# Performance work log

Hardware: AMD Instinct MI355X
Metric: run time of the kernel (lower is better)

Reference implementation:

```python
import jax, jax.numpy as jnp
import numpy as np

P_SIZE = 13
B_THRESH = 1.3  # |u| >= b -> hard 1.0
N_POW = 64      # u^n / (u^n + 1)


def make_dct_weight(p):
    idx = np.arange(p)
    Ci = np.where(idx == 0, 1.0 / np.sqrt(2.0), 1.0)
    cos = np.cos((2 * idx[:, None] + 1) * idx[None, :] * np.pi / (2 * p)) * Ci[None, :]  # [x,i]
    P = (2.0 / p) * np.einsum('xi,yj->xyij', cos, cos).reshape(p * p, p * p)
    return P.T.astype(np.float32).reshape(p * p, 1, p, p)


def conv2d(x, w, padding):
    return jax.lax.conv_general_dilated(x, w, (1, 1), padding,
                                        dimension_numbers=('NCHW', 'OIHW', 'NCHW'))


def udiff(u):
    # x^64/(x^64+1), saturated to 1 for |x| >= 1.3 (even power, sign-safe)
    au = jnp.abs(u)
    us = jnp.where(au < B_THRESH, u, 0.0)  # avoid overflow in pow
    y = us ** N_POW
    return jnp.where(au >= B_THRESH, jnp.ones_like(u), y / (y + 1.0))


def setup_inputs() -> dict:
    key = jax.random.key(0)
    k1, _ = jax.random.split(key)
    x = jax.random.uniform(k1, (2, 1, 512, 512), dtype=jnp.float32)
    sigma = jnp.full((1,), 0.1, dtype=jnp.float32)
    W_dct = jnp.asarray(make_dct_weight(P_SIZE))  # [p^2, 1, p, p], learnable in original
    return {"x": x, "sigma": sigma, "W_dct": W_dct}


def reference(x, sigma, W_dct):
    N, _, H, W = x.shape
    p = W_dct.shape[-1]
    pp = p * p
    # patch DCT: [N, p^2, H-p+1, W-p+1]
    t = conv2d(x, W_dct, 'VALID')
    nz = udiff(t / (3.0 * sigma))
    y = t * nz
    w = 1.0 / (1.0 + jnp.sum(nz, axis=1, keepdims=True))  # [N,1,H',W']
    # inverse transform as 1x1 conv with inv(dct matrix)
    Minv = jnp.linalg.inv(W_dct.reshape(pp, pp))
    z = jnp.einsum('kc,nchw->nkhw', Minv, y)
    z = w * z
    # overlap-add fold == conv with spatially-flipped identity patch kernel, full padding
    fold_k = jnp.flip(jnp.eye(pp, dtype=x.dtype).reshape(pp, p, p), axis=(1, 2))[None]  # [1,p^2,p,p]
    folded = conv2d(z, fold_k, [(p - 1, p - 1), (p - 1, p - 1)])  # [N,1,H,W]
    out = folded[:, :, p - 1:H - (p - 1), p - 1:W - (p - 1)]
    divisor = conv2d(w, jnp.ones((1, 1, p, p), x.dtype), 'VALID')
    return out / divisor
```

## Files before the change

kernel.cpp:

```cpp
#include <hip/hip_runtime.h>
#include <math.h>


#define P13    13
#define IMGW   512
#define OUTW   488
#define SEGH   31
#define NSEG   16
#define HCOLS  512
#define HPITCH 16

struct C1mat { float v[P13 * P13]; };

constexpr double kPI = 3.14159265358979323846264338327950288;

constexpr double ccos_pm_pi(double th) {
    double term = 1.0, s = 1.0;
    const double th2 = th * th;
    for (int n = 1; n <= 25; ++n) {
        term *= -th2 / (double)((2 * n - 1) * (2 * n));
        s += term;
    }
    return s;
}
constexpr double csqrt(double v) {
    double x = (v > 1.0) ? v : 1.0;
    for (int i = 0; i < 64; ++i) x = 0.5 * (x + v / x);
    return x;
}
constexpr C1mat make_c1() {
    C1mat m{};
    const double s213 = csqrt(2.0 / 13.0);
    const double is2  = 1.0 / csqrt(2.0);
    for (int x = 0; x < P13; ++x)
        for (int k = 0; k < P13; ++k) {
            int mm = ((2 * x + 1) * k) % 52;
            double th = (mm <= 26) ? (mm * kPI / 26.0) : ((mm - 52) * kPI / 26.0);
            double Ci = (k == 0) ? is2 : 1.0;
            m.v[x * P13 + k] = (float)(s213 * Ci * ccos_pm_pi(th));
        }
    return m;
}
__device__ constexpr C1mat c1c = make_c1();

struct FalseT { static constexpr bool value = false; };
struct TrueT  { static constexpr bool value = true; };

#define ROR16_ADD(v, N)                                                        \
    v += __int_as_float(__builtin_amdgcn_mov_dpp(__float_as_int(v),            \
                                                 0x120 + (N), 0xF, 0xF, true))

__device__ __forceinline__ void vdct_shrink(const float (&Rv)[P13],
                                            float inv3s, float (&tn)[P13], float& pnz)
{
    float Se[6], So[6];
#pragma unroll
    for (int k = 0; k < 6; ++k) { Se[k] = Rv[k] + Rv[12 - k]; So[k] = Rv[k] - Rv[12 - k]; }
#pragma unroll
    for (int i = 0; i < P13; ++i) {
        float t;
        if ((i & 1) == 0) {
            t = c1c.v[6 * P13 + i] * Rv[6];
#pragma unroll
            for (int k = 0; k < 6; ++k) t = fmaf(c1c.v[k * P13 + i], Se[k], t);
        } else {
            t = c1c.v[0 * P13 + i] * So[0];
#pragma unroll
            for (int k = 1; k < 6; ++k) t = fmaf(c1c.v[k * P13 + i], So[k], t);
        }
        float u = t * inv3s;
        float lg = __builtin_amdgcn_logf(fabsf(u));
        float q  = __builtin_amdgcn_exp2f(-64.0f * lg);
        float nz = __builtin_amdgcn_rcpf(1.0f + q);
        pnz += nz;
        tn[i] = t * nz;
    }
}

__device__ __forceinline__ void fold_vert(const float (&tn)[P13], float w1, float (&H)[P13])
{
#pragma unroll
    for (int dx = 0; dx < 6; ++dx) {
        float E = c1c.v[dx * P13 + 0] * tn[0];
#pragma unroll
        for (int i = 2; i < P13; i += 2) E = fmaf(c1c.v[dx * P13 + i], tn[i], E);
        float O = c1c.v[dx * P13 + 1] * tn[1];
#pragma unroll
        for (int i = 3; i < P13; i += 2) O = fmaf(c1c.v[dx * P13 + i], tn[i], O);
        H[dx]      = fmaf(w1, E + O, H[dx]);
        H[12 - dx] = fmaf(w1, E - O, H[12 - dx]);
    }
    float z6 = c1c.v[6 * P13 + 0] * tn[0];
#pragma unroll
    for (int i = 2; i < P13; i += 2) z6 = fmaf(c1c.v[6 * P13 + i], tn[i], z6);
    H[6] = fmaf(w1, z6, H[6]);
}

__global__ __launch_bounds__(256) void dct2net_k2(
    const float* __restrict__ xg, const float* __restrict__ sigmag,
    float* __restrict__ Hg, float* __restrict__ Wg)
{
    __shared__ float c1lds[169];
    const int tid = threadIdx.x;
    if (tid < 169) c1lds[tid] = c1c.v[tid];
    __syncthreads();

    const int lane = tid & 63;
    const int wv   = tid >> 6;
    const int g    = lane >> 4;
    const int jj   = lane & 15;
    const int img  = blockIdx.z;
    const int hs   = blockIdx.y * SEGH;
    const int segrows = (OUTW - hs < SEGH) ? (OUTW - hs) : SEGH;
    const int cbw  = blockIdx.x * 16 + wv * 4;
    const int col  = cbw + g;

    const float inv3s = 1.0f / (3.0f * sigmag[0]);
    const float* xin  = xg + (size_t)img * IMGW * IMGW;

    float c1col[P13];
    {
        const int jc = (jj < 13) ? jj : 12;
#pragma unroll
        for (int y = 0; y < P13; ++y) c1col[y] = c1lds[y * P13 + jc];
    }

    float Rv[P13], Hr[P13], wr[12];
#pragma unroll
    for (int k = 0; k < P13; ++k) { Rv[k] = 0.0f; Hr[k] = 0.0f; }
#pragma unroll
    for (int k = 0; k < 12; ++k) wr[k] = 0.0f;
    float vs = 0.0f;

    int xcol = cbw + lane; xcol = (xcol < IMGW - 1) ? xcol : (IMGW - 1);
    float xv = 0.0f;
    if (lane < 16) xv = xin[(size_t)hs * IMGW + xcol];

    auto step = [&](int k, auto SH, auto RT) {
        float xw[P13];
#pragma unroll
        for (int y = 0; y < P13; ++y)
            xw[y] = __int_as_float(
                __builtin_amdgcn_ds_bpermute(4 * (g + y), __float_as_int(xv)));
        {
            int nr = hs + k + 1; nr = (nr < IMGW) ? nr : (IMGW - 1);
            if (lane < 16) xv = xin[(size_t)nr * IMGW + xcol];
        }
        float a0 = c1col[0] * xw[0], a1 = c1col[1] * xw[1];
#pragma unroll
        for (int y = 2; y < P13; y += 2) a0 = fmaf(c1col[y], xw[y], a0);
#pragma unroll
        for (int y = 3; y < P13; y += 2) a1 = fmaf(c1col[y], xw[y], a1);
#pragma unroll
        for (int q = 0; q < P13 - 1; ++q) Rv[q] = Rv[q + 1];
        Rv[P13 - 1] = a0 + a1;

        if constexpr (decltype(SH)::value) {
            float tn[P13]; float pnz = 0.0f;
            vdct_shrink(Rv, inv3s, tn, pnz);
            if (jj >= 13) pnz = 0.0f;
            ROR16_ADD(pnz, 1);
            ROR16_ADD(pnz, 2);
            ROR16_ADD(pnz, 4);
            ROR16_ADD(pnz, 8);
            const float w = __builtin_amdgcn_rcpf(1.0f + pnz);
            vs += w;
            fold_vert(tn, w, Hr);
            if constexpr (decltype(RT)::value) {
                const int a = hs + k - 24;
                Hg[(((size_t)img * OUTW + a) * HCOLS + col) * HPITCH + jj] = Hr[0];
                if (jj == 0) Wg[((size_t)img * IMGW + a) * IMGW + col] = vs;
                vs -= wr[0];
            }
#pragma unroll
            for (int q = 0; q < 11; ++q) wr[q] = wr[q + 1];
            wr[11] = w;
#pragma unroll
            for (int q = 0; q < P13 - 1; ++q) Hr[q] = Hr[q + 1];
            Hr[P13 - 1] = 0.0f;
        }
    };

#pragma unroll 4
    for (int k = 0; k < 12; ++k) step(k, FalseT{}, FalseT{});
#pragma unroll 4
    for (int k = 12; k < 24; ++k) step(k, TrueT{}, FalseT{});
    const int kend = 24 + segrows;
#pragma unroll 4
    for (int k = 24; k < kend; ++k) step(k, TrueT{}, TrueT{});
}

__global__ __launch_bounds__(256) void dct2net_k3(
    const float* __restrict__ Hg, const float* __restrict__ Wg,
    float* __restrict__ outg)
{
    __shared__ float U[4][76][14];
    __shared__ float vw[4][80];
    const int tid  = threadIdx.x;
    const int lane = tid & 63;
    const int wv   = tid >> 6;
    const int img  = blockIdx.z;
    const int a    = blockIdx.y * 4 + wv;
    const int cb   = blockIdx.x * 64;

#pragma unroll
    for (int h = 0; h < 2; ++h) {
        const int li = lane + 64 * h;
        if (h == 0 || lane < 12) {
            int c = cb + li; c = (c < 499) ? c : 499;
            const float* hp = &Hg[(((size_t)img * OUTW + a) * HCOLS + c) * HPITCH];
            float hv[P13];
            *(float4*)&hv[0] = *(const float4*)hp;
            *(float4*)&hv[4] = *(const float4*)(hp + 4);
            *(float4*)&hv[8] = *(const float4*)(hp + 8);
            hv[12] = hp[12];
            vw[wv][li] = Wg[((size_t)img * IMGW + a) * IMGW + c];
#pragma unroll
            for (int dy = 0; dy < P13; ++dy) {
                float s0 = c1c.v[dy * P13 + 0] * hv[0];
                float s1 = c1c.v[dy * P13 + 1] * hv[1];
#pragma unroll
                for (int j = 2; j < P13; j += 2) s0 = fmaf(c1c.v[dy * P13 + j], hv[j], s0);
#pragma unroll
                for (int j = 3; j < P13; j += 2) s1 = fmaf(c1c.v[dy * P13 + j], hv[j], s1);
                U[wv][li][dy] = s0 + s1;
            }
        }
    }
    float num = 0.0f;
#pragma unroll
    for (int dy = 0; dy < P13; ++dy) num += U[wv][lane + 12 - dy][dy];
    float den = 0.0f;
#pragma unroll
    for (int d = 0; d < P13; ++d) den += vw[wv][lane + d];
    const int ow = cb + lane;
    if (ow < OUTW)
        outg[((size_t)img * OUTW + a) * OUTW + ow] = num * __builtin_amdgcn_rcpf(den);
}

extern "C" void kernel_launch(void* const* d_in, const int* in_sizes, int n_in,
                              void* d_out, int out_size, void* d_ws, size_t ws_size,
                              hipStream_t stream)
{
    const float* x     = (const float*)d_in[0];
    const float* sigma = (const float*)d_in[1];
    float* out = (float*)d_out;

    float* Hg = (float*)d_ws;
    float* Wg = Hg + (size_t)2 * OUTW * HCOLS * HPITCH;

    dct2net_k2<<<dim3(32, NSEG, 2), 256, 0, stream>>>(x, sigma, Hg, Wg);
    dct2net_k3<<<dim3(8, 122, 2), 256, 0, stream>>>(Hg, Wg, out);
}
```

Measured before the change: 179.9 us.

## Rotate register rings, square-power shrink, 64-thread k2 blocks, spread k3 halo

Kernel k2 now runs as single-wave blocks with taller segments. The steady-state loop is unrolled 13 times with compile-time rotating register indices, so the per-row shift of the Rv/Hr/wr arrays goes away, and pointers advance incrementally. The shrink function replaces log/exp2 with repeated squaring of t^2/(9s^2), clamped at 1.69, and computes 1-nz directly. In k3, the 12-column halo work is spread across 48 threads instead of making lanes 0-11 of every wave do two passes, and a __syncthreads is added. Risks include higher register pressure, a different numerical path for the shrink weight, and fewer halo-recompute segments being traded for fewer, larger blocks.

```diff
diff --git a/kernel.cpp b/kernel.cpp
--- a/kernel.cpp
+++ b/kernel.cpp
@@ -5,8 +5,8 @@
 #define P13    13
 #define IMGW   512
 #define OUTW   488
-#define SEGH   31
-#define NSEG   16
+#define SEGH   39
+#define NSEG   13
 #define HCOLS  512
 #define HPITCH 16
 
@@ -50,17 +50,22 @@
     v += __int_as_float(__builtin_amdgcn_mov_dpp(__float_as_int(v),            \
                                                  0x120 + (N), 0xF, 0xF, true))
 
-__device__ __forceinline__ void vdct_shrink(const float (&Rv)[P13],
-                                            float inv3s, float (&tn)[P13], float& pnz)
+template<int RO>
+__device__ __forceinline__ void vdct_shrink_r(const float (&Rv)[P13], float i2sq,
+                                              float (&tn)[P13], float& pnzr)
 {
     float Se[6], So[6];
 #pragma unroll
-    for (int k = 0; k < 6; ++k) { Se[k] = Rv[k] + Rv[12 - k]; So[k] = Rv[k] - Rv[12 - k]; }
+    for (int k = 0; k < 6; ++k) {
+        float a = Rv[(k + RO) % P13], b = Rv[(12 - k + RO) % P13];
+        Se[k] = a + b; So[k] = a - b;
+    }
+    const float R6v = Rv[(6 + RO) % P13];
 #pragma unroll
     for (int i = 0; i < P13; ++i) {
         float t;
         if ((i & 1) == 0) {
-            t = c1c.v[6 * P13 + i] * Rv[6];
+            t = c1c.v[6 * P13 + i] * R6v;
 #pragma unroll
             for (int k = 0; k < 6; ++k) t = fmaf(c1c.v[k * P13 + i], Se[k], t);
         } else {
@@ -68,16 +73,17 @@
 #pragma unroll
             for (int k = 1; k < 6; ++k) t = fmaf(c1c.v[k * P13 + i], So[k], t);
         }
-        float u = t * inv3s;
-        float lg = __builtin_amdgcn_logf(fabsf(u));
-        float q  = __builtin_amdgcn_exp2f(-64.0f * lg);
-        float nz = __builtin_amdgcn_rcpf(1.0f + q);
-        pnz += nz;
-        tn[i] = t * nz;
-    }
-}
-
-__device__ __forceinline__ void fold_vert(const float (&tn)[P13], float w1, float (&H)[P13])
+        float p2 = fminf(t * t * i2sq, 1.69f);
+        float p4 = p2 * p2, p8 = p4 * p4, p16 = p8 * p8, p32 = p16 * p16, p64 = p32 * p32;
+        float r  = __builtin_amdgcn_rcpf(p64 + 1.0f);
+        pnzr += r;
+        tn[i] = fmaf(-t, r, t);
+    }
+}
+
+template<int R>
+__device__ __forceinline__ void fold_vert_r(const float (&tn)[P13], float w1,
+                                            float (&H)[P13])
 {
 #pragma unroll
     for (int dx = 0; dx < 6; ++dx) {
@@ -87,65 +93,105 @@
         float O = c1c.v[dx * P13 + 1] * tn[1];
 #pragma unroll
         for (int i = 3; i < P13; i += 2) O = fmaf(c1c.v[dx * P13 + i], tn[i], O);
-        H[dx]      = fmaf(w1, E + O, H[dx]);
-        H[12 - dx] = fmaf(w1, E - O, H[12 - dx]);
+        H[(dx + R) % P13]      = fmaf(w1, E + O, H[(dx + R) % P13]);
+        H[(12 - dx + R) % P13] = fmaf(w1, E - O, H[(12 - dx + R) % P13]);
     }
     float z6 = c1c.v[6 * P13 + 0] * tn[0];
 #pragma unroll
     for (int i = 2; i < P13; i += 2) z6 = fmaf(c1c.v[6 * P13 + i], tn[i], z6);
-    H[6] = fmaf(w1, z6, H[6]);
-}
-
-__global__ __launch_bounds__(256) void dct2net_k2(
+    H[(6 + R) % P13] = fmaf(w1, z6, H[(6 + R) % P13]);
+}
+
+template<int R>
+__device__ __forceinline__ void k2_sub(
+    float (&Rv)[P13], float (&Hr)[P13], float (&wr)[P13],
+    float& vs, float& xv, const float*& xp, const float* xlast, int xcol,
+    const float (&c1col)[P13], int g, int jj, float i2sq,
+    float*& Hp, float*& Wp, int voH, int voW)
+{
+    float xw[P13];
+#pragma unroll
+    for (int y = 0; y < P13; ++y)
+        xw[y] = __int_as_float(
+            __builtin_amdgcn_ds_bpermute(4 * (g + y), __float_as_int(xv)));
+    {
+        const float* xq = (xp < xlast) ? xp : xlast;
+        xv = xq[xcol]; xp += IMGW;
+    }
+    float a0 = c1col[0] * xw[0], a1 = c1col[1] * xw[1];
+#pragma unroll
+    for (int y = 2; y < P13; y += 2) a0 = fmaf(c1col[y], xw[y], a0);
+#pragma unroll
+    for (int y = 3; y < P13; y += 2) a1 = fmaf(c1col[y], xw[y], a1);
+    Rv[R] = a0 + a1;
+
+    float tn[P13]; float pnzr = 0.0f;
+    vdct_shrink_r<(R + 1) % P13>(Rv, i2sq, tn, pnzr);
+    float pnz = 13.0f - pnzr;
+    ROR16_ADD(pnz, 1); ROR16_ADD(pnz, 2); ROR16_ADD(pnz, 4); ROR16_ADD(pnz, 8);
+    const float w = __builtin_amdgcn_rcpf(1.0f + pnz);
+    vs += w;
+    fold_vert_r<R>(tn, w, Hr);
+    wr[R] = w;
+    Hp[voH] = Hr[R];
+    Hp += HCOLS * HPITCH;
+    if (jj == 0) Wp[voW] = vs;
+    Wp += IMGW;
+    vs -= wr[(R + 1) % P13];
+    Hr[R] = 0.0f;
+}
+
+__global__ __launch_bounds__(64) void dct2net_k2(
     const float* __restrict__ xg, const float* __restrict__ sigmag,
     float* __restrict__ Hg, float* __restrict__ Wg)
 {
     __shared__ float c1lds[169];
     const int tid = threadIdx.x;
-    if (tid < 169) c1lds[tid] = c1c.v[tid];
-    __syncthreads();
-
-    const int lane = tid & 63;
-    const int wv   = tid >> 6;
+    c1lds[tid] = c1c.v[tid];
+    c1lds[tid + 64] = c1c.v[tid + 64];
+    if (tid < 41) c1lds[tid + 128] = c1c.v[tid + 128];
+
+    const int lane = tid;
     const int g    = lane >> 4;
     const int jj   = lane & 15;
     const int img  = blockIdx.z;
     const int hs   = blockIdx.y * SEGH;
     const int segrows = (OUTW - hs < SEGH) ? (OUTW - hs) : SEGH;
-    const int cbw  = blockIdx.x * 16 + wv * 4;
+    const int cbw  = blockIdx.x * 4;
     const int col  = cbw + g;
 
     const float inv3s = 1.0f / (3.0f * sigmag[0]);
+    const float i2sq  = inv3s * inv3s;
     const float* xin  = xg + (size_t)img * IMGW * IMGW;
 
     float c1col[P13];
-    {
-        const int jc = (jj < 13) ? jj : 12;
-#pragma unroll
-        for (int y = 0; y < P13; ++y) c1col[y] = c1lds[y * P13 + jc];
-    }
-
-    float Rv[P13], Hr[P13], wr[12];
-#pragma unroll
-    for (int k = 0; k < P13; ++k) { Rv[k] = 0.0f; Hr[k] = 0.0f; }
-#pragma unroll
-    for (int k = 0; k < 12; ++k) wr[k] = 0.0f;
+#pragma unroll
+    for (int y = 0; y < P13; ++y)
+        c1col[y] = (jj < 13) ? c1lds[y * P13 + jj] : 0.0f;
+
+    float Rv[P13], Hr[P13], wr[P13];
+#pragma unroll
+    for (int k = 0; k < P13; ++k) { Rv[k] = 0.0f; Hr[k] = 0.0f; wr[k] = 0.0f; }
     float vs = 0.0f;
 
-    int xcol = cbw + lane; xcol = (xcol < IMGW - 1) ? xcol : (IMGW - 1);
-    float xv = 0.0f;
-    if (lane < 16) xv = xin[(size_t)hs * IMGW + xcol];
-
-    auto step = [&](int k, auto SH, auto RT) {
+    int xcol = cbw + (lane & 15); xcol = (xcol < IMGW - 1) ? xcol : (IMGW - 1);
+    const float* xp    = xin + (size_t)hs * IMGW;
+    const float* xlast = xin + (size_t)(IMGW - 1) * IMGW;
+    float xv = xp[xcol];
+    xp += IMGW;
+
+    float* Hp = Hg + ((size_t)img * OUTW + hs) * HCOLS * HPITCH;
+    float* Wp = Wg + ((size_t)img * IMGW + hs) * IMGW;
+    const int voH = col * HPITCH + jj;
+    const int voW = col;
+
+    auto stepS = [&](auto SH, auto RT) {
         float xw[P13];
 #pragma unroll
         for (int y = 0; y < P13; ++y)
             xw[y] = __int_as_float(
                 __builtin_amdgcn_ds_bpermute(4 * (g + y), __float_as_int(xv)));
-        {
-            int nr = hs + k + 1; nr = (nr < IMGW) ? nr : (IMGW - 1);
-            if (lane < 16) xv = xin[(size_t)nr * IMGW + xcol];
-        }
+        { const float* xq = (xp < xlast) ? xp : xlast; xv = xq[xcol]; xp += IMGW; }
         float a0 = c1col[0] * xw[0], a1 = c1col[1] * xw[1];
 #pragma unroll
         for (int y = 2; y < P13; y += 2) a0 = fmaf(c1col[y], xw[y], a0);
@@ -156,38 +202,46 @@
         Rv[P13 - 1] = a0 + a1;
 
         if constexpr (decltype(SH)::value) {
-            float tn[P13]; float pnz = 0.0f;
-            vdct_shrink(Rv, inv3s, tn, pnz);
-            if (jj >= 13) pnz = 0.0f;
-            ROR16_ADD(pnz, 1);
-            ROR16_ADD(pnz, 2);
-            ROR16_ADD(pnz, 4);
-            ROR16_ADD(pnz, 8);
+            float tn[P13]; float pnzr = 0.0f;
+            vdct_shrink_r<0>(Rv, i2sq, tn, pnzr);
+            float pnz = 13.0f - pnzr;
+            ROR16_ADD(pnz, 1); ROR16_ADD(pnz, 2); ROR16_ADD(pnz, 4); ROR16_ADD(pnz, 8);
             const float w = __builtin_amdgcn_rcpf(1.0f + pnz);
             vs += w;
-            fold_vert(tn, w, Hr);
+            fold_vert_r<0>(tn, w, Hr);
+#pragma unroll
+            for (int q = 0; q < P13 - 1; ++q) wr[q] = wr[q + 1];
+            wr[P13 - 1] = w;
             if constexpr (decltype(RT)::value) {
-                const int a = hs + k - 24;
-                Hg[(((size_t)img * OUTW + a) * HCOLS + col) * HPITCH + jj] = Hr[0];
-                if (jj == 0) Wg[((size_t)img * IMGW + a) * IMGW + col] = vs;
+                Hp[voH] = Hr[0];
+                Hp += HCOLS * HPITCH;
+                if (jj == 0) Wp[voW] = vs;
+                Wp += IMGW;
                 vs -= wr[0];
             }
 #pragma unroll
-            for (int q = 0; q < 11; ++q) wr[q] = wr[q + 1];
-            wr[11] = w;
-#pragma unroll
             for (int q = 0; q < P13 - 1; ++q) Hr[q] = Hr[q + 1];
             Hr[P13 - 1] = 0.0f;
         }
     };
 
-#pragma unroll 4
-    for (int k = 0; k < 12; ++k) step(k, FalseT{}, FalseT{});
-#pragma unroll 4
-    for (int k = 12; k < 24; ++k) step(k, TrueT{}, FalseT{});
-    const int kend = 24 + segrows;
-#pragma unroll 4
-    for (int k = 24; k < kend; ++k) step(k, TrueT{}, TrueT{});
+#pragma unroll 1
+    for (int k = 0; k < 12; ++k) stepS(FalseT{}, FalseT{});
+#pragma unroll 1
+    for (int k = 0; k < 12; ++k) stepS(TrueT{}, FalseT{});
+
+#define SUB(R) k2_sub<R>(Rv, Hr, wr, vs, xv, xp, xlast, xcol, c1col, g, jj, \
+                         i2sq, Hp, Wp, voH, voW)
+    int kleft = segrows;
+#pragma unroll 1
+    while (kleft >= 13) {
+        SUB(0); SUB(1); SUB(2); SUB(3); SUB(4); SUB(5); SUB(6);
+        SUB(7); SUB(8); SUB(9); SUB(10); SUB(11); SUB(12);
+        kleft -= 13;
+    }
+#undef SUB
+#pragma unroll 1
+    for (; kleft > 0; --kleft) stepS(TrueT{}, TrueT{});
 }
 
 __global__ __launch_bounds__(256) void dct2net_k3(
@@ -200,33 +254,66 @@
     const int lane = tid & 63;
     const int wv   = tid >> 6;
     const int img  = blockIdx.z;
-    const int a    = blockIdx.y * 4 + wv;
+    const int a0   = blockIdx.y * 4;
+    const int a    = a0 + wv;
     const int cb   = blockIdx.x * 64;
 
-#pragma unroll
-    for (int h = 0; h < 2; ++h) {
-        const int li = lane + 64 * h;
-        if (h == 0 || lane < 12) {
-            int c = cb + li; c = (c < 499) ? c : 499;
-            const float* hp = &Hg[(((size_t)img * OUTW + a) * HCOLS + c) * HPITCH];
-            float hv[P13];
-            *(float4*)&hv[0] = *(const float4*)hp;
-            *(float4*)&hv[4] = *(const float4*)(hp + 4);
-            *(float4*)&hv[8] = *(const float4*)(hp + 8);
-            hv[12] = hp[12];
-            vw[wv][li] = Wg[((size_t)img * IMGW + a) * IMGW + c];
-#pragma unroll
-            for (int dy = 0; dy < P13; ++dy) {
-                float s0 = c1c.v[dy * P13 + 0] * hv[0];
-                float s1 = c1c.v[dy * P13 + 1] * hv[1];
-#pragma unroll
-                for (int j = 2; j < P13; j += 2) s0 = fmaf(c1c.v[dy * P13 + j], hv[j], s0);
-#pragma unroll
-                for (int j = 3; j < P13; j += 2) s1 = fmaf(c1c.v[dy * P13 + j], hv[j], s1);
-                U[wv][li][dy] = s0 + s1;
-            }
-        }
-    }
+    int c = cb + lane; c = (c < 499) ? c : 499;
+    const float* hp = &Hg[(((size_t)img * OUTW + a) * HCOLS + c) * HPITCH];
+    float4 m0 = *(const float4*)hp;
+    float4 m1 = *(const float4*)(hp + 4);
+    float4 m2 = *(const float4*)(hp + 8);
+    float  m3 = hp[12];
+    float  wm = Wg[((size_t)img * IMGW + a) * IMGW + c];
+
+    const bool halo = (tid < 48);
+    const int  hr = tid / 12;
+    const int  hm = tid - hr * 12;
+    float4 s0 = {0,0,0,0}, s1 = {0,0,0,0}, s2 = {0,0,0,0};
+    float  s3 = 0.0f, ws = 0.0f;
+    if (halo) {
+        const int ah = a0 + hr;
+        int c2 = cb + 64 + hm; c2 = (c2 < 499) ? c2 : 499;
+        const float* hq = &Hg[(((size_t)img * OUTW + ah) * HCOLS + c2) * HPITCH];
+        s0 = *(const float4*)hq;
+        s1 = *(const float4*)(hq + 4);
+        s2 = *(const float4*)(hq + 8);
+        s3 = hq[12];
+        ws = Wg[((size_t)img * IMGW + ah) * IMGW + c2];
+    }
+
+    {
+        float hv[P13] = {m0.x,m0.y,m0.z,m0.w, m1.x,m1.y,m1.z,m1.w,
+                         m2.x,m2.y,m2.z,m2.w, m3};
+#pragma unroll
+        for (int dy = 0; dy < P13; ++dy) {
+            float u0 = c1c.v[dy * P13 + 0] * hv[0];
+            float u1 = c1c.v[dy * P13 + 1] * hv[1];
+#pragma unroll
+            for (int j = 2; j < P13; j += 2) u0 = fmaf(c1c.v[dy * P13 + j], hv[j], u0);
+#pragma unroll
+            for (int j = 3; j < P13; j += 2) u1 = fmaf(c1c.v[dy * P13 + j], hv[j], u1);
+            U[wv][lane][dy] = u0 + u1;
+        }
+        vw[wv][lane] = wm;
+    }
+    if (halo) {
+        float hv[P13] = {s0.x,s0.y,s0.z,s0.w, s1.x,s1.y,s1.z,s1.w,
+                         s2.x,s2.y,s2.z,s2.w, s3};
+#pragma unroll
+        for (int dy = 0; dy < P13; ++dy) {
+            float u0 = c1c.v[dy * P13 + 0] * hv[0];
+            float u1 = c1c.v[dy * P13 + 1] * hv[1];
+#pragma unroll
+            for (int j = 2; j < P13; j += 2) u0 = fmaf(c1c.v[dy * P13 + j], hv[j], u0);
+#pragma unroll
+            for (int j = 3; j < P13; j += 2) u1 = fmaf(c1c.v[dy * P13 + j], hv[j], u1);
+            U[hr][64 + hm][dy] = u0 + u1;
+        }
+        vw[hr][64 + hm] = ws;
+    }
+    __syncthreads();
+
     float num = 0.0f;
 #pragma unroll
     for (int dy = 0; dy < P13; ++dy) num += U[wv][lane + 12 - dy][dy];
@@ -249,6 +336,6 @@
     float* Hg = (float*)d_ws;
     float* Wg = Hg + (size_t)2 * OUTW * HCOLS * HPITCH;
 
-    dct2net_k2<<<dim3(32, NSEG, 2), 256, 0, stream>>>(x, sigma, Hg, Wg);
+    dct2net_k2<<<dim3(128, NSEG, 2), 64, 0, stream>>>(x, sigma, Hg, Wg);
     dct2net_k3<<<dim3(8, 122, 2), 256, 0, stream>>>(Hg, Wg, out);
 }
```

Result: slower. 236.6 us (+31.6%).
